# Kernel optimization log

Hardware: AMD Instinct MI355X
Metric: run time of the kernel (lower is better)

## Reference

```python
import jax, jax.numpy as jnp
import numpy as np


def setup_inputs() -> dict:
    key = jax.random.key(0)
    k1, k2, k3, k4 = jax.random.split(key, 4)
    B, D, N, M = 4, 256, 4096, 4096
    return {
        "src": jax.random.normal(k1, (B, 3, N), dtype=jnp.float32),
        "tgt": jax.random.normal(k2, (B, 3, M), dtype=jnp.float32),
        "src_emb": jax.random.normal(k3, (B, D, N), dtype=jnp.float32),
        "tgt_emb": jax.random.normal(k4, (B, D, M), dtype=jnp.float32),
    }


def reference(src, tgt, src_emb, tgt_emb):
    # pairwise_distance[b,n,m] = -||src_emb[:,n] - tgt_emb[:,m]||^2
    # decomposed as -xx + 2*inner - yy (inner below is -2*dot, as in torch code)
    inner = -2.0 * jnp.einsum("bdn,bdm->bnm", src_emb, tgt_emb)       # [B,N,M]
    xx = jnp.sum(src_emb ** 2, axis=1)[:, :, None]                     # [B,N,1]
    yy = jnp.sum(tgt_emb ** 2, axis=1)[:, None, :]                     # [B,1,M]
    pairwise_distance = -xx - inner - yy                               # [B,N,M]
    scores = jax.nn.softmax(pairwise_distance, axis=2)                 # softmax over tgt points
    # src_corr[b,c,n] = sum_m tgt[b,c,m] * scores[b,n,m]
    src_corr = jnp.einsum("bcm,bnm->bcn", tgt, scores)                 # [B,3,N]
    return src_corr
```

## Files before the change

kernel.cpp:

```cpp
#include <hip/hip_runtime.h>

#define NBATCH 4
#define DDIM   256
#define NN     4096
#define MM     4096
#define NCHUNK 8
#define MCHUNK 512
#define MTILE  64
#define LOG2E  1.44269504088896340736f

using half8   = __attribute__((ext_vector_type(8))) _Float16;
using floatx4 = __attribute__((ext_vector_type(4))) float;

__global__ __launch_bounds__(256) void k_prep(const float* __restrict__ src_emb,
                                              const float* __restrict__ tgt_emb,
                                              _Float16* __restrict__ Qh,
                                              _Float16* __restrict__ Kh) {
    __shared__ float tile[64][65];
    int bz = blockIdx.z;
    int tensor = bz >> 2, b = bz & 3;
    const float* in = tensor ? tgt_emb : src_emb;
    _Float16* out   = tensor ? Kh : Qh;
    const float scale = tensor ? 1.0f : 2.0f * LOG2E;
    int n0 = blockIdx.x * 64, d0 = blockIdx.y * 64;
    int t = threadIdx.x;
    {
        int c = t & 63, r0 = t >> 6;
        const float* ip = in + (size_t)(b * DDIM + d0) * NN + n0 + c;
#pragma unroll
        for (int i = 0; i < 16; i++) {
            int r = r0 + i * 4;
            tile[r][c] = ip[(size_t)r * NN];
        }
    }
    __syncthreads();
    int dg = t & 7, nn = t >> 3;
#pragma unroll
    for (int pass = 0; pass < 2; pass++) {
        int n = nn + pass * 32;
        half8 h;
#pragma unroll
        for (int k = 0; k < 8; k++) h[k] = (_Float16)(tile[dg * 8 + k][n] * scale);
        *(half8*)(out + (size_t)(b * NN + n0 + n) * DDIM + d0 + dg * 8) = h;
    }
}

__global__ __launch_bounds__(256) void k_yy(const _Float16* __restrict__ Kh,
                                            float* __restrict__ yy) {
    int b = blockIdx.y;
    int m = blockIdx.x * 64 + (threadIdx.x >> 2);
    int j = threadIdx.x & 3;
    const half8* p = (const half8*)(Kh + (size_t)(b * MM + m) * DDIM);
    float s = 0.f;
#pragma unroll
    for (int k = 0; k < 8; k++) {
        half8 v = p[k * 4 + j];
#pragma unroll
        for (int e = 0; e < 8; e++) { float f = (float)v[e]; s = fmaf(f, f, s); }
    }
    s += __shfl_xor(s, 1, 64);
    s += __shfl_xor(s, 2, 64);
    if (j == 0) yy[b * MM + m] = s * (-LOG2E);
}

__global__ __launch_bounds__(256, 2) void k_flash(const _Float16* __restrict__ Qh,
                                                  const _Float16* __restrict__ Kh,
                                                  const float* __restrict__ yy,
                                                  const float* __restrict__ tgt,
                                                  float4* __restrict__ Opart,
                                                  float* __restrict__ Mpart) {
    __shared__ half8   Kt8[MTILE * 33];
    __shared__ floatx4 yyt4[MTILE / 4];
    __shared__ floatx4 vtt[MTILE];

    int i = blockIdx.x;
    int xcd = i & 7, s = i >> 3;
    int grp = xcd + 8 * (s >> 4);
    int b = grp >> 3, chunk = grp & 7, ntile = s & 15;

    int t = threadIdx.x, wave = t >> 6, lane = t & 63, quad = lane >> 4, l15 = lane & 15;
    int n0 = ntile * 256 + wave * 64;

    const half8* qp = (const half8*)Qh + (size_t)b * NN * 32;
    half8 qf[4][8];
#pragma unroll
    for (int nb = 0; nb < 4; nb++) {
        int n = n0 + nb * 16 + l15;
#pragma unroll
        for (int ds = 0; ds < 8; ds++) qf[nb][ds] = qp[n * 32 + ds * 4 + quad];
    }

    const floatx4 z4 = {0.f, 0.f, 0.f, 0.f};
    floatx4 o[4] = {z4, z4, z4, z4};
    float mr[4] = {-__builtin_inff(), -__builtin_inff(), -__builtin_inff(), -__builtin_inff()};

    const half8* kp = (const half8*)Kh + (size_t)b * MM * 32;
    const float* tb = tgt + (size_t)b * 3 * MM;
    int m0 = chunk * MCHUNK;
    int srow = t >> 5, sdc = t & 31;

    for (int mt = 0; mt < MCHUNK / MTILE; mt++) {
        int mg = m0 + mt * MTILE;
        __syncthreads();
#pragma unroll
        for (int it = 0; it < 8; it++) {
            int mrow = srow + it * 8;
            Kt8[mrow * 33 + sdc] = kp[(size_t)(mg + mrow) * 32 + sdc];
        }
        if (t < MTILE) {
            int m = mg + t;
            floatx4 v = {tb[m], tb[MM + m], tb[2 * MM + m], 1.0f};
            vtt[t] = v;
        } else if (t < MTILE + MTILE / 4) {
            yyt4[t - MTILE] = ((const floatx4*)(yy + b * MM + mg))[t - MTILE];
        }
        __syncthreads();

        floatx4 acc[4][4];
#pragma unroll
        for (int nb = 0; nb < 4; nb++)
#pragma unroll
            for (int mb = 0; mb < 4; mb++) acc[nb][mb] = z4;
#pragma unroll
        for (int ds = 0; ds < 8; ds++) {
            half8 a[4];
#pragma unroll
            for (int mb = 0; mb < 4; mb++) a[mb] = Kt8[(mb * 16 + l15) * 33 + ds * 4 + quad];
#pragma unroll
            for (int nb = 0; nb < 4; nb++)
#pragma unroll
                for (int mb = 0; mb < 4; mb++)
                    acc[nb][mb] = __builtin_amdgcn_mfma_f32_16x16x32_f16(a[mb], qf[nb][ds], acc[nb][mb], 0, 0, 0);
        }

#pragma unroll
        for (int mb = 0; mb < 4; mb++) {
            floatx4 yv = yyt4[mb * 4 + quad];
#pragma unroll
            for (int nb = 0; nb < 4; nb++) acc[nb][mb] = acc[nb][mb] + yv;
        }
#pragma unroll
        for (int nb = 0; nb < 4; nb++) {
            floatx4 mx = __builtin_elementwise_max(
                __builtin_elementwise_max(acc[nb][0], acc[nb][1]),
                __builtin_elementwise_max(acc[nb][2], acc[nb][3]));
            float tm = fmaxf(fmaxf(mx[0], mx[1]), fmaxf(mx[2], mx[3]));
            tm = fmaxf(tm, __shfl_xor(tm, 16, 64));
            tm = fmaxf(tm, __shfl_xor(tm, 32, 64));
            float mn = fmaxf(mr[nb], tm);
            float al = __builtin_amdgcn_exp2f(mr[nb] - mn);
            mr[nb] = mn;
            o[nb] = o[nb] * al;
            floatx4 mnv = {mn, mn, mn, mn};
#pragma unroll
            for (int mb = 0; mb < 4; mb++) acc[nb][mb] = acc[nb][mb] - mnv;
        }
#pragma unroll
        for (int mb = 0; mb < 4; mb++) {
            floatx4 vr[4];
#pragma unroll
            for (int r = 0; r < 4; r++) vr[r] = vtt[mb * 16 + quad * 4 + r];
#pragma unroll
            for (int nb = 0; nb < 4; nb++)
#pragma unroll
                for (int r = 0; r < 4; r++) {
                    float p = __builtin_amdgcn_exp2f(acc[nb][mb][r]);
                    o[nb] = o[nb] + p * vr[r];
                }
        }
    }

#pragma unroll
    for (int nb = 0; nb < 4; nb++) {
#pragma unroll
        for (int c = 0; c < 4; c++) {
            float v = o[nb][c];
            v += __shfl_xor(v, 16, 64);
            v += __shfl_xor(v, 32, 64);
            o[nb][c] = v;
        }
    }
    if (quad == 0) {
#pragma unroll
        for (int nb = 0; nb < 4; nb++) {
            int n = n0 + nb * 16 + l15;
            size_t idx = (size_t)(chunk * NBATCH + b) * NN + n;
            Opart[idx] = make_float4(o[nb][0], o[nb][1], o[nb][2], o[nb][3]);
            Mpart[idx] = mr[nb];
        }
    }
}

__global__ __launch_bounds__(256) void k_combine(const float4* __restrict__ Opart,
                                                 const float* __restrict__ Mpart,
                                                 float* __restrict__ out) {
    int idx = blockIdx.x * 256 + threadIdx.x;
    int b = idx >> 12, n = idx & (NN - 1);
    float mstar = -__builtin_inff();
#pragma unroll
    for (int j = 0; j < NCHUNK; j++)
        mstar = fmaxf(mstar, Mpart[(size_t)(j * NBATCH + b) * NN + n]);
    float o0 = 0.f, o1 = 0.f, o2 = 0.f, l = 0.f;
#pragma unroll
    for (int j = 0; j < NCHUNK; j++) {
        size_t id = (size_t)(j * NBATCH + b) * NN + n;
        float w = __builtin_amdgcn_exp2f(Mpart[id] - mstar);
        float4 P = Opart[id];
        o0 = fmaf(w, P.x, o0); o1 = fmaf(w, P.y, o1);
        o2 = fmaf(w, P.z, o2); l  = fmaf(w, P.w, l);
    }
    out[(size_t)(b * 3 + 0) * NN + n] = o0 / l;
    out[(size_t)(b * 3 + 1) * NN + n] = o1 / l;
    out[(size_t)(b * 3 + 2) * NN + n] = o2 / l;
}

extern "C" void kernel_launch(void* const* d_in, const int* in_sizes, int n_in,
                              void* d_out, int out_size, void* d_ws, size_t ws_size,
                              hipStream_t stream) {
    const float* tgt     = (const float*)d_in[1];
    const float* src_emb = (const float*)d_in[2];
    const float* tgt_emb = (const float*)d_in[3];
    float* out = (float*)d_out;

    char* ws = (char*)d_ws;
    _Float16* Qh = (_Float16*)(ws);
    _Float16* Kh = (_Float16*)(ws + 8388608);
    float*    yy = (float*)   (ws + 16777216);
    float4*   Op = (float4*)  (ws + 16842752);
    float*    Mp = (float*)   (ws + 18939904);

    hipLaunchKernelGGL(k_prep,    dim3(64, 4, 8), dim3(256), 0, stream, src_emb, tgt_emb, Qh, Kh);
    hipLaunchKernelGGL(k_yy,      dim3(64, 4),    dim3(256), 0, stream, Kh, yy);
    hipLaunchKernelGGL(k_flash,   dim3(512),      dim3(256), 0, stream, Qh, Kh, yy, tgt, Op, Mp);
    hipLaunchKernelGGL(k_combine, dim3(64),       dim3(256), 0, stream, Op, Mp, out);
}
```

Baseline: 141.5 us.

## Double-buffer K tiles via direct global-to-LDS loads and fuse yy into prep

The flash kernel now stages each K tile straight into a double-buffered, XOR-swizzled LDS buffer with global_load_lds, so the next tile loads while MFMAs run on the current one. yy and the tgt value vectors are read straight from global memory instead of LDS. The per-tile cross-quad max shuffle is replaced by per-lane running maxima that are merged once at the end. The prep kernel now also computes yy (in fp32, from the unrounded inputs) and packs tgt into float4, which removes the separate yy kernel; the combine kernel launches more, smaller blocks. In exchange, LDS use grows to 64 KB per block and the prep kernel's grid shrinks to 512 blocks, each handling a full 256-wide tile.

```diff
diff --git a/kernel.cpp b/kernel.cpp
--- a/kernel.cpp
+++ b/kernel.cpp
@@ -7,6 +7,7 @@
 #define NCHUNK 8
 #define MCHUNK 512
 #define MTILE  64
+#define NT     (MCHUNK / MTILE)
 #define LOG2E  1.44269504088896340736f
 
 using half8   = __attribute__((ext_vector_type(8))) _Float16;
@@ -14,72 +15,72 @@
 
 __global__ __launch_bounds__(256) void k_prep(const float* __restrict__ src_emb,
                                               const float* __restrict__ tgt_emb,
+                                              const float* __restrict__ tgt,
                                               _Float16* __restrict__ Qh,
-                                              _Float16* __restrict__ Kh) {
-    __shared__ float tile[64][65];
-    int bz = blockIdx.z;
-    int tensor = bz >> 2, b = bz & 3;
+                                              _Float16* __restrict__ Kh,
+                                              float* __restrict__ yyS,
+                                              float4* __restrict__ Vt) {
+    __shared__ float tile[64][257];
+    __shared__ float psum[8][64];
+    int bz = blockIdx.z, tensor = bz >> 2, b = bz & 3;
     const float* in = tensor ? tgt_emb : src_emb;
-    _Float16* out   = tensor ? Kh : Qh;
+    _Float16* out = tensor ? Kh : Qh;
     const float scale = tensor ? 1.0f : 2.0f * LOG2E;
-    int n0 = blockIdx.x * 64, d0 = blockIdx.y * 64;
+    int n0 = blockIdx.x * 64;
     int t = threadIdx.x;
-    {
-        int c = t & 63, r0 = t >> 6;
-        const float* ip = in + (size_t)(b * DDIM + d0) * NN + n0 + c;
-#pragma unroll
-        for (int i = 0; i < 16; i++) {
-            int r = r0 + i * 4;
-            tile[r][c] = ip[(size_t)r * NN];
-        }
-    }
+
+    int c2 = t & 31, part = t >> 5;
+    const float* ip = in + (size_t)(b * DDIM + part) * NN + n0 + c2 * 2;
+    float s0 = 0.f, s1 = 0.f;
+#pragma unroll
+    for (int i = 0; i < 32; i++) {
+        float2 v = *(const float2*)(ip + (size_t)(i * 8) * NN);
+        tile[c2 * 2][part + i * 8]     = v.x;
+        tile[c2 * 2 + 1][part + i * 8] = v.y;
+        s0 = fmaf(v.x, v.x, s0);
+        s1 = fmaf(v.y, v.y, s1);
+    }
+    if (tensor) { psum[part][c2 * 2] = s0; psum[part][c2 * 2 + 1] = s1; }
     __syncthreads();
-    int dg = t & 7, nn = t >> 3;
-#pragma unroll
-    for (int pass = 0; pass < 2; pass++) {
-        int n = nn + pass * 32;
+
+    int dg = t & 31, nn = t >> 5;
+#pragma unroll
+    for (int p = 0; p < 8; p++) {
+        int n = p * 8 + nn;
+        const float* row = &tile[n][dg * 8];
         half8 h;
 #pragma unroll
-        for (int k = 0; k < 8; k++) h[k] = (_Float16)(tile[dg * 8 + k][n] * scale);
-        *(half8*)(out + (size_t)(b * NN + n0 + n) * DDIM + d0 + dg * 8) = h;
-    }
-}
-
-__global__ __launch_bounds__(256) void k_yy(const _Float16* __restrict__ Kh,
-                                            float* __restrict__ yy) {
-    int b = blockIdx.y;
-    int m = blockIdx.x * 64 + (threadIdx.x >> 2);
-    int j = threadIdx.x & 3;
-    const half8* p = (const half8*)(Kh + (size_t)(b * MM + m) * DDIM);
-    float s = 0.f;
-#pragma unroll
-    for (int k = 0; k < 8; k++) {
-        half8 v = p[k * 4 + j];
-#pragma unroll
-        for (int e = 0; e < 8; e++) { float f = (float)v[e]; s = fmaf(f, f, s); }
-    }
-    s += __shfl_xor(s, 1, 64);
-    s += __shfl_xor(s, 2, 64);
-    if (j == 0) yy[b * MM + m] = s * (-LOG2E);
+        for (int k = 0; k < 8; k++) h[k] = (_Float16)(row[k] * scale);
+        *(half8*)(out + (size_t)(b * NN + n0 + n) * DDIM + dg * 8) = h;
+    }
+    if (tensor && t < 64) {
+        float s = 0.f;
+#pragma unroll
+        for (int j = 0; j < 8; j++) s += psum[j][t];
+        int m = n0 + t;
+        yyS[b * MM + m] = s * (-LOG2E);
+        Vt[(size_t)b * MM + m] = make_float4(tgt[(size_t)b * 3 * MM + m],
+                                             tgt[(size_t)b * 3 * MM + MM + m],
+                                             tgt[(size_t)b * 3 * MM + 2 * MM + m], 1.0f);
+    }
 }
 
 __global__ __launch_bounds__(256, 2) void k_flash(const _Float16* __restrict__ Qh,
                                                   const _Float16* __restrict__ Kh,
-                                                  const float* __restrict__ yy,
-                                                  const float* __restrict__ tgt,
+                                                  const float* __restrict__ yyS,
+                                                  const float4* __restrict__ Vt,
                                                   float4* __restrict__ Opart,
                                                   float* __restrict__ Mpart) {
-    __shared__ half8   Kt8[MTILE * 33];
-    __shared__ floatx4 yyt4[MTILE / 4];
-    __shared__ floatx4 vtt[MTILE];
+    __shared__ __align__(16) _Float16 Kt[2][MTILE * DDIM];
 
     int i = blockIdx.x;
-    int xcd = i & 7, s = i >> 3;
-    int grp = xcd + 8 * (s >> 4);
-    int b = grp >> 3, chunk = grp & 7, ntile = s & 15;
+    int xcd = i & 7, sb = i >> 3;
+    int grp = xcd + 8 * (sb >> 4);
+    int b = grp >> 3, chunk = grp & 7, ntile = sb & 15;
 
     int t = threadIdx.x, wave = t >> 6, lane = t & 63, quad = lane >> 4, l15 = lane & 15;
     int n0 = ntile * 256 + wave * 64;
+    int m0 = chunk * MCHUNK;
 
     const half8* qp = (const half8*)Qh + (size_t)b * NN * 32;
     half8 qf[4][8];
@@ -90,42 +91,59 @@
         for (int ds = 0; ds < 8; ds++) qf[nb][ds] = qp[n * 32 + ds * 4 + quad];
     }
 
+    const _Float16* kp = Kh + (size_t)b * MM * DDIM;
+    int ssl = lane & 31, shalf = lane >> 5;
+    auto stage = [&](int mt) {
+        const _Float16* gb = kp + (size_t)(m0 + mt * MTILE + wave * 16) * DDIM;
+        _Float16* lb = &Kt[mt & 1][wave * 16 * DDIM];
+#pragma unroll
+        for (int it = 0; it < 8; it++) {
+            int rl = it * 2 + shalf;
+            int rloc = wave * 16 + rl;
+            int g = (ssl & 24) | ((ssl ^ rloc) & 7);
+            const _Float16* gp = gb + (size_t)rl * DDIM + g * 8;
+            __builtin_amdgcn_global_load_lds(
+                (const __attribute__((address_space(1))) uint32_t*)(const void*)gp,
+                (__attribute__((address_space(3))) uint32_t*)(void*)(lb + it * 2 * DDIM),
+                16, 0, 0);
+        }
+    };
+
     const floatx4 z4 = {0.f, 0.f, 0.f, 0.f};
     floatx4 o[4] = {z4, z4, z4, z4};
-    float mr[4] = {-__builtin_inff(), -__builtin_inff(), -__builtin_inff(), -__builtin_inff()};
-
-    const half8* kp = (const half8*)Kh + (size_t)b * MM * 32;
-    const float* tb = tgt + (size_t)b * 3 * MM;
-    int m0 = chunk * MCHUNK;
-    int srow = t >> 5, sdc = t & 31;
-
-    for (int mt = 0; mt < MCHUNK / MTILE; mt++) {
-        int mg = m0 + mt * MTILE;
+    float mr[4];
+#pragma unroll
+    for (int nb = 0; nb < 4; nb++) mr[nb] = -__builtin_inff();
+
+    const float* yb = yyS + (size_t)b * MM;
+    const float4* vb = Vt + (size_t)b * MM;
+    int r7 = l15 & 7;
+
+    stage(0);
+    for (int mt = 0; mt < NT; mt++) {
         __syncthreads();
-#pragma unroll
-        for (int it = 0; it < 8; it++) {
-            int mrow = srow + it * 8;
-            Kt8[mrow * 33 + sdc] = kp[(size_t)(mg + mrow) * 32 + sdc];
-        }
-        if (t < MTILE) {
-            int m = mg + t;
-            floatx4 v = {tb[m], tb[MM + m], tb[2 * MM + m], 1.0f};
-            vtt[t] = v;
-        } else if (t < MTILE + MTILE / 4) {
-            yyt4[t - MTILE] = ((const floatx4*)(yy + b * MM + mg))[t - MTILE];
-        }
-        __syncthreads();
-
+
+        int jb = m0 + mt * MTILE + quad * 4;
+        floatx4 yv[4];
+#pragma unroll
+        for (int mb = 0; mb < 4; mb++) yv[mb] = *(const floatx4*)(yb + jb + mb * 16);
+
+        if (mt + 1 < NT) stage(mt + 1);
+
+        const _Float16* Kb = &Kt[mt & 1][0];
         floatx4 acc[4][4];
 #pragma unroll
         for (int nb = 0; nb < 4; nb++)
 #pragma unroll
             for (int mb = 0; mb < 4; mb++) acc[nb][mb] = z4;
+
 #pragma unroll
         for (int ds = 0; ds < 8; ds++) {
+            int slot = (ds * 4 + quad) ^ r7;
             half8 a[4];
 #pragma unroll
-            for (int mb = 0; mb < 4; mb++) a[mb] = Kt8[(mb * 16 + l15) * 33 + ds * 4 + quad];
+            for (int mb = 0; mb < 4; mb++)
+                a[mb] = *(const half8*)(Kb + (size_t)(mb * 16 + l15) * DDIM + slot * 8);
 #pragma unroll
             for (int nb = 0; nb < 4; nb++)
 #pragma unroll
@@ -134,19 +152,13 @@
         }
 
 #pragma unroll
-        for (int mb = 0; mb < 4; mb++) {
-            floatx4 yv = yyt4[mb * 4 + quad];
-#pragma unroll
-            for (int nb = 0; nb < 4; nb++) acc[nb][mb] = acc[nb][mb] + yv;
-        }
-#pragma unroll
         for (int nb = 0; nb < 4; nb++) {
+#pragma unroll
+            for (int mb = 0; mb < 4; mb++) acc[nb][mb] = acc[nb][mb] + yv[mb];
             floatx4 mx = __builtin_elementwise_max(
                 __builtin_elementwise_max(acc[nb][0], acc[nb][1]),
                 __builtin_elementwise_max(acc[nb][2], acc[nb][3]));
             float tm = fmaxf(fmaxf(mx[0], mx[1]), fmaxf(mx[2], mx[3]));
-            tm = fmaxf(tm, __shfl_xor(tm, 16, 64));
-            tm = fmaxf(tm, __shfl_xor(tm, 32, 64));
             float mn = fmaxf(mr[nb], tm);
             float al = __builtin_amdgcn_exp2f(mr[nb] - mn);
             mr[nb] = mn;
@@ -157,28 +169,39 @@
         }
 #pragma unroll
         for (int mb = 0; mb < 4; mb++) {
-            floatx4 vr[4];
-#pragma unroll
-            for (int r = 0; r < 4; r++) vr[r] = vtt[mb * 16 + quad * 4 + r];
-#pragma unroll
-            for (int nb = 0; nb < 4; nb++)
-#pragma unroll
-                for (int r = 0; r < 4; r++) {
-                    float p = __builtin_amdgcn_exp2f(acc[nb][mb][r]);
-                    o[nb] = o[nb] + p * vr[r];
-                }
+            const float4* vp = vb + jb + mb * 16;
+            float4 v0 = vp[0], v1 = vp[1], v2 = vp[2], v3 = vp[3];
+#pragma unroll
+            for (int nb = 0; nb < 4; nb++) {
+                floatx4 pa;
+#pragma unroll
+                for (int r = 0; r < 4; r++) pa[r] = __builtin_amdgcn_exp2f(acc[nb][mb][r]);
+                floatx4 oo = o[nb];
+                oo += pa[0] * (floatx4){v0.x, v0.y, v0.z, v0.w};
+                oo += pa[1] * (floatx4){v1.x, v1.y, v1.z, v1.w};
+                oo += pa[2] * (floatx4){v2.x, v2.y, v2.z, v2.w};
+                oo += pa[3] * (floatx4){v3.x, v3.y, v3.z, v3.w};
+                o[nb] = oo;
+            }
         }
     }
 
 #pragma unroll
     for (int nb = 0; nb < 4; nb++) {
+        float mq = mr[nb];
+        float ma = fmaxf(mq, __shfl_xor(mq, 16, 64));
+        ma = fmaxf(ma, __shfl_xor(ma, 32, 64));
+        float w = __builtin_amdgcn_exp2f(mq - ma);
+        floatx4 ow = o[nb] * w;
 #pragma unroll
         for (int c = 0; c < 4; c++) {
-            float v = o[nb][c];
+            float v = ow[c];
             v += __shfl_xor(v, 16, 64);
             v += __shfl_xor(v, 32, 64);
-            o[nb][c] = v;
-        }
+            ow[c] = v;
+        }
+        o[nb] = ow;
+        mr[nb] = ma;
     }
     if (quad == 0) {
 #pragma unroll
@@ -191,10 +214,10 @@
     }
 }
 
-__global__ __launch_bounds__(256) void k_combine(const float4* __restrict__ Opart,
+__global__ __launch_bounds__(128) void k_combine(const float4* __restrict__ Opart,
                                                  const float* __restrict__ Mpart,
                                                  float* __restrict__ out) {
-    int idx = blockIdx.x * 256 + threadIdx.x;
+    int idx = blockIdx.x * 128 + threadIdx.x;
     int b = idx >> 12, n = idx & (NN - 1);
     float mstar = -__builtin_inff();
 #pragma unroll
@@ -223,14 +246,15 @@
     float* out = (float*)d_out;
 
     char* ws = (char*)d_ws;
-    _Float16* Qh = (_Float16*)(ws);
-    _Float16* Kh = (_Float16*)(ws + 8388608);
-    float*    yy = (float*)   (ws + 16777216);
-    float4*   Op = (float4*)  (ws + 16842752);
-    float*    Mp = (float*)   (ws + 18939904);
-
-    hipLaunchKernelGGL(k_prep,    dim3(64, 4, 8), dim3(256), 0, stream, src_emb, tgt_emb, Qh, Kh);
-    hipLaunchKernelGGL(k_yy,      dim3(64, 4),    dim3(256), 0, stream, Kh, yy);
-    hipLaunchKernelGGL(k_flash,   dim3(512),      dim3(256), 0, stream, Qh, Kh, yy, tgt, Op, Mp);
-    hipLaunchKernelGGL(k_combine, dim3(64),       dim3(256), 0, stream, Op, Mp, out);
-}
+    _Float16* Qh  = (_Float16*)(ws);
+    _Float16* Kh  = (_Float16*)(ws + 8388608);
+    float*    yyS = (float*)   (ws + 16777216);
+    float4*   Vt  = (float4*)  (ws + 16842752);
+    float4*   Op  = (float4*)  (ws + 17104896);
+    float*    Mp  = (float*)   (ws + 19202048);
+
+    hipLaunchKernelGGL(k_prep,    dim3(64, 1, 8), dim3(256), 0, stream,
+                       src_emb, tgt_emb, tgt, Qh, Kh, yyS, Vt);
+    hipLaunchKernelGGL(k_flash,   dim3(512),      dim3(256), 0, stream, Qh, Kh, yyS, Vt, Op, Mp);
+    hipLaunchKernelGGL(k_combine, dim3(128),      dim3(128), 0, stream, Op, Mp, out);
+}
```

Measured after the change: 148.4 us. 1.05x slower.
